# Kernel tuning notes

Measured on AMD Instinct MI355X. Metric: run time of the kernel, lower is better.

## Reference

```python
import jax, jax.numpy as jnp
import numpy as np

B, N, C, K3, KNN = 4, 4096, 128, 3, 16
SCALE = 1.0 / np.sqrt(C)  # attention uses sqrt(embed_dim)
EPS = 1e-5


def _knn_idx(x, k):
    # squared euclidean distances (monotone in cdist), topk smallest
    x2 = jnp.sum(x * x, axis=-1)                       # [B,N]
    d2 = x2[:, :, None] + x2[:, None, :] - 2.0 * jnp.einsum('bnd,bmd->bnm', x, x)
    _, idx = jax.lax.top_k(-d2, k)                     # [B,N,k]
    return idx


def _gather(x, idx):
    # knn_gather: x [B,N,D], idx [B,N,k] -> [B,N,k,D]
    return jax.vmap(lambda xb, ib: xb[ib])(x, idx)


def _attn(q_in, kv_in, Wq, Wk, Wv):
    # q_in [B,N,D], kv_in [B,N,k,D]; torch Linear: x @ W.T
    Q = q_in @ Wq.T
    Kt = kv_in @ Wk.T
    V = kv_in @ Wv.T
    scores = jnp.einsum('bnkd,bnd->bnk', Kt, Q) * SCALE
    a = jax.nn.softmax(scores, axis=-1)
    return jnp.einsum('bnk,bnkd->bnd', a, V)


def _ln(x, g, b):
    mu = jnp.mean(x, axis=-1, keepdims=True)
    var = jnp.mean((x - mu) ** 2, axis=-1, keepdims=True)
    return (x - mu) * jax.lax.rsqrt(var + EPS) * g + b


def setup_inputs() -> dict:
    key = jax.random.key(0)
    ks = jax.random.split(key, 20)
    s = 0.05
    inp = {
        'src': jax.random.normal(ks[0], (B, N, K3), dtype=jnp.float32),
        'tgt': jax.random.normal(ks[1], (B, N, C), dtype=jnp.float32),
        'Wq0': jax.random.normal(ks[2], (C, C), dtype=jnp.float32) * s,
        'Wk0': jax.random.normal(ks[3], (C, C), dtype=jnp.float32) * s,
        'Wv0': jax.random.normal(ks[4], (C, C), dtype=jnp.float32) * s,
        'Wq1': jax.random.normal(ks[5], (C, C), dtype=jnp.float32) * s,
        'Wk1': jax.random.normal(ks[6], (C, C), dtype=jnp.float32) * s,
        'Wv1': jax.random.normal(ks[7], (C, C), dtype=jnp.float32) * s,
        'Wp0': jax.random.normal(ks[8], (C, K3), dtype=jnp.float32) * s,
        'bp0': jnp.zeros((C,), dtype=jnp.float32),
        'Wp1': jax.random.normal(ks[9], (C, C), dtype=jnp.float32) * s,
        'bp1': jnp.zeros((C,), dtype=jnp.float32),
        'Wl': jax.random.normal(ks[10], (C, C), dtype=jnp.float32) * s,
        'bl': jnp.zeros((C,), dtype=jnp.float32),
        'g0': jnp.ones((C,), dtype=jnp.float32),
        'b0': jnp.zeros((C,), dtype=jnp.float32),
        'g1': jnp.ones((C,), dtype=jnp.float32),
        'b1': jnp.zeros((C,), dtype=jnp.float32),
    }
    return inp


def reference(src, tgt, Wq0, Wk0, Wv0, Wq1, Wk1, Wv1, Wp0, bp0, Wp1, bp1, Wl, bl, g0, b0, g1, b1):
    k = min(KNN, src.shape[1])
    # stage 1: knn on coordinates
    idx = _knn_idx(src, k)
    gather_src = _gather(src, idx)                         # [B,N,k,3]
    residual_src = (src[:, :, None, :] - gather_src) @ Wp0.T + bp0
    gather_tgt = _gather(tgt, idx)                         # [B,N,k,C]
    out = _attn(tgt, residual_src + gather_tgt, Wq0, Wk0, Wv0)
    # stage 2: knn in feature space
    idx2 = _knn_idx(out, k)
    gather_out = _gather(out, idx2)
    residual_out = (out[:, :, None, :] - gather_out) @ Wp1.T + bp1
    out = _attn(out, residual_out + gather_out, Wq1, Wk1, Wv1)
    out_0 = tgt + out
    out_1 = _ln(out_0, g0, b0) @ Wl.T + bl
    out_2 = _ln(tgt + out_1, g1, b1)
    return jnp.transpose(out_2, (1, 0, 2))                 # [N,B,C]
```

## Files before the change

kernel.cpp:

```cpp
#include <hip/hip_runtime.h>
#include <math.h>

#define NB 4
#define NN 4096
#define NC 128
#define NROWS (NB*NN)
#define SCALE_F 0.08838834764831845f

using bf16x8 = __attribute__((ext_vector_type(8))) short;
using f32x4  = __attribute__((ext_vector_type(4))) float;

__device__ __forceinline__ float rl_f(float x, int l) {
    return __int_as_float(__builtin_amdgcn_readlane(__float_as_int(x), l));
}
__device__ __forceinline__ ushort f2bf(float x) {
    unsigned u = __float_as_uint(x);
    return (ushort)((u + 0x7FFF + ((u >> 16) & 1)) >> 16);
}
__device__ __forceinline__ float bf2f(ushort b) { return __uint_as_float(((unsigned)b) << 16); }

__device__ __forceinline__ unsigned long long mkkey(float d2, int idx) {
    unsigned u = __float_as_uint(d2);
    u ^= ((unsigned)((int)u >> 31)) | 0x80000000u;
    return ((unsigned long long)u << 32) | (unsigned)idx;
}

#define DECL16V \
    float v0=INFINITY,v1=INFINITY,v2=INFINITY,v3=INFINITY,v4=INFINITY,v5=INFINITY,v6=INFINITY,v7=INFINITY, \
          v8=INFINITY,v9=INFINITY,v10=INFINITY,v11=INFINITY,v12=INFINITY,v13=INFINITY,v14=INFINITY,v15=INFINITY;

#define INSERT16V(dv) do { float d_=(dv); \
    bool m0=d_<v0,m1=d_<v1,m2=d_<v2,m3=d_<v3,m4=d_<v4,m5=d_<v5,m6=d_<v6,m7=d_<v7, \
         m8=d_<v8,m9=d_<v9,m10=d_<v10,m11=d_<v11,m12=d_<v12,m13=d_<v13,m14=d_<v14,m15=d_<v15; \
    v15=m14?v14:(m15?d_:v15); v14=m13?v13:(m14?d_:v14); v13=m12?v12:(m13?d_:v13); v12=m11?v11:(m12?d_:v12); \
    v11=m10?v10:(m11?d_:v11); v10=m9?v9:(m10?d_:v10); v9 =m8?v8:(m9?d_:v9);  v8 =m7?v7:(m8?d_:v8); \
    v7 =m6?v6:(m7?d_:v7);   v6 =m5?v5:(m6?d_:v6);   v5 =m4?v4:(m5?d_:v5);  v4 =m3?v3:(m4?d_:v4); \
    v3 =m2?v2:(m3?d_:v3);   v2 =m1?v1:(m2?d_:v2);   v1 =m0?v0:(m1?d_:v1);  v0 =m0?d_:v0; } while(0)

#define POP16V(p) do { bool p_=(p); \
    v0=p_?v1:v0; v1=p_?v2:v1; v2=p_?v3:v2; v3=p_?v4:v3; v4=p_?v5:v4; v5=p_?v6:v5; v6=p_?v7:v6; v7=p_?v8:v7; \
    v8=p_?v9:v8; v9=p_?v10:v9; v10=p_?v11:v10; v11=p_?v12:v11; v12=p_?v13:v12; v13=p_?v14:v13; v14=p_?v15:v14; \
    v15=p_?INFINITY:v15; } while(0)

#define KMAX16 0xFFFFFFFFFFFFFFFFull
#define DECL16K \
    unsigned long long K0=KMAX16,K1=KMAX16,K2=KMAX16,K3=KMAX16,K4=KMAX16,K5=KMAX16,K6=KMAX16,K7=KMAX16, \
                       K8=KMAX16,K9=KMAX16,K10=KMAX16,K11=KMAX16,K12=KMAX16,K13=KMAX16,K14=KMAX16,K15=KMAX16;

#define INSERT16K(kv) do { unsigned long long k_=(kv); \
    bool m0=k_<K0,m1=k_<K1,m2=k_<K2,m3=k_<K3,m4=k_<K4,m5=k_<K5,m6=k_<K6,m7=k_<K7, \
         m8=k_<K8,m9=k_<K9,m10=k_<K10,m11=k_<K11,m12=k_<K12,m13=k_<K13,m14=k_<K14,m15=k_<K15; \
    K15=m14?K14:(m15?k_:K15); K14=m13?K13:(m14?k_:K14); K13=m12?K12:(m13?k_:K13); K12=m11?K11:(m12?k_:K12); \
    K11=m10?K10:(m11?k_:K11); K10=m9?K9:(m10?k_:K10);   K9 =m8?K8:(m9?k_:K9);    K8 =m7?K7:(m8?k_:K8); \
    K7 =m6?K6:(m7?k_:K7);     K6 =m5?K5:(m6?k_:K6);     K5 =m4?K4:(m5?k_:K5);    K4 =m3?K3:(m4?k_:K4); \
    K3 =m2?K2:(m3?k_:K3);     K2 =m1?K1:(m2?k_:K2);     K1 =m0?K0:(m1?k_:K1);    K0 =m0?k_:K0; } while(0)

#define POP16K(p) do { bool p_=(p); \
    K0=p_?K1:K0; K1=p_?K2:K1; K2=p_?K3:K2; K3=p_?K4:K3; K4=p_?K5:K4; K5=p_?K6:K5; K6=p_?K7:K6; K7=p_?K8:K7; \
    K8=p_?K9:K8; K9=p_?K10:K9; K10=p_?K11:K10; K11=p_?K12:K11; K12=p_?K13:K12; K13=p_?K14:K13; K14=p_?K15:K14; \
    K15=p_?KMAX16:K15; } while(0)

__global__ void combo_small(const float* __restrict__ Wk0, const float* __restrict__ Wv0,
                            const float* __restrict__ Wp0, const float* __restrict__ bp0,
                            float* __restrict__ WKP0, float* __restrict__ BK0,
                            float* __restrict__ WVP0, float* __restrict__ BV0)
{
    int task = blockIdx.x * 512 + threadIdx.x;
    if (task >= 1024) return;
    int mat = task >> 9; int rem = task & 511;
    int c = rem >> 2, t = rem & 3;
    const float* W = mat ? Wv0 : Wk0;
    float s = 0.f;
    if (t < 3) {
        for (int d = 0; d < 128; ++d) s = fmaf(W[c*128+d], Wp0[d*3+t], s);
        (mat ? WVP0 : WKP0)[c*3+t] = s;
    } else {
        for (int d = 0; d < 128; ++d) s = fmaf(W[c*128+d], bp0[d], s);
        (mat ? BV0 : BK0)[c] = s;
    }
}

__global__ void combo_big(const float* __restrict__ Wk1, const float* __restrict__ Wv1,
                          const float* __restrict__ Wp1, const float* __restrict__ bp1,
                          float* __restrict__ WKD, float* __restrict__ MV1,
                          float* __restrict__ WVD, float* __restrict__ BV1)
{
    int task = blockIdx.x * 256 + threadIdx.x;
    if (task >= 32896) return;
    if (task < 32768) {
        int mat = task >> 14; int rem = task & 16383;
        int c = rem >> 7, tcol = rem & 127;
        const float* W = mat ? Wv1 : Wk1;
        float s = 0.f;
        for (int d = 0; d < 128; ++d) s = fmaf(W[c*128+d], Wp1[d*128+tcol], s);
        if (mat) { MV1[rem] = s; WVD[rem] = Wv1[rem] - s; }
        else     { WKD[rem] = Wk1[rem] - s; }
    } else {
        int c = task - 32768;
        float s = 0.f;
        for (int d = 0; d < 128; ++d) s = fmaf(Wv1[c*128+d], bp1[d], s);
        BV1[c] = s;
    }
}

__global__ void srcproj(const float* __restrict__ src, const float* __restrict__ WKP0,
                        const float* __restrict__ WVP0,
                        float* __restrict__ srcKp, float* __restrict__ srcVp)
{
    int gid = blockIdx.x * 256 + threadIdx.x;
    int i = gid >> 7, c = gid & 127;
    float s0 = src[i*3+0], s1 = src[i*3+1], s2 = src[i*3+2];
    srcKp[gid] = fmaf(s0, WKP0[c*3+0], fmaf(s1, WKP0[c*3+1], s2*WKP0[c*3+2]));
    srcVp[gid] = fmaf(s0, WVP0[c*3+0], fmaf(s1, WVP0[c*3+1], s2*WVP0[c*3+2]));
}

__global__ __launch_bounds__(256) void knn1_kernel(const float* __restrict__ src,
                                                   int* __restrict__ idxout)
{
    int lane = threadIdx.x & 63, wave = threadIdx.x >> 6;
    int b7 = blockIdx.x & 7, sub = blockIdx.x >> 3;
    int batch = b7 >> 1;
    int rib = (sub*2 + (b7 & 1))*4 + wave;
    int row = batch*NN + rib;
    const float* sb = src + batch*NN*3;
    float xi0 = sb[rib*3], xi1 = sb[rib*3+1], xi2 = sb[rib*3+2];

    DECL16V
    for (int it = 0; it < 64; ++it) {
        int j = it*64 + lane;
        float dx = xi0 - sb[j*3], dy = xi1 - sb[j*3+1], dz = xi2 - sb[j*3+2];
        float d2 = fmaf(dx, dx, fmaf(dy, dy, dz*dz));
        if (d2 < v15) INSERT16V(d2);
    }
    float T = INFINITY;
    for (int t = 0; t < 16; ++t) {
        float g = v0;
#pragma unroll
        for (int off = 1; off < 64; off <<= 1) g = fminf(g, __shfl_xor(g, off, 64));
        unsigned long long b = __ballot(v0 == g);
        int f = __ffsll((long long)b) - 1;
        POP16V(lane == f);
        T = g;
    }
    unsigned long long below_mask = (lane == 63) ? 0x7fffffffffffffffull : ((1ull << lane) - 1ull);
    int base = 0;
    for (int it = 0; it < 64; ++it) {
        int j = it*64 + lane;
        float dx = xi0 - sb[j*3], dy = xi1 - sb[j*3+1], dz = xi2 - sb[j*3+2];
        float d2 = fmaf(dx, dx, fmaf(dy, dy, dz*dz));
        unsigned long long blt = __ballot(d2 < T);
        if (d2 < T) idxout[row*16 + base + __popcll(blt & below_mask)] = j;
        base += __popcll(blt);
    }
    for (int it = 0; it < 64 && base < 16; ++it) {
        int j = it*64 + lane;
        float dx = xi0 - sb[j*3], dy = xi1 - sb[j*3+1], dz = xi2 - sb[j*3+2];
        float d2 = fmaf(dx, dx, fmaf(dy, dy, dz*dz));
        unsigned long long beq = __ballot(d2 == T);
        int bel = __popcll(beq & below_mask);
        if (d2 == T && base + bel < 16) idxout[row*16 + base + bel] = j;
        base += __popcll(beq);
    }
}

__device__ __forceinline__ void matmul128_body(const float* __restrict__ X,
                                               const float* __restrict__ W,
                                               const float* __restrict__ S,
                                               float* __restrict__ Y)
{
    __shared__ float WL[128*128];
    int tid = threadIdx.x;
    for (int f = tid; f < 16384; f += 256) {
        int c = f >> 7, d = f & 127;
        WL[d*128 + (c ^ (d & 14))] = W[f];
    }
    __syncthreads();
    int lane = tid & 63, wave = tid >> 6;
#pragma unroll
    for (int it = 0; it < 2; ++it) {
        int row0 = blockIdx.x*32 + it*16 + wave*4;
        float x0[4], x1[4];
#pragma unroll
        for (int r = 0; r < 4; ++r) {
            x0[r] = X[(row0+r)*128 + lane];
            x1[r] = X[(row0+r)*128 + lane + 64];
        }
        float2 acc[4];
#pragma unroll
        for (int r = 0; r < 4; ++r) { acc[r].x = 0.f; acc[r].y = 0.f; }
#pragma unroll 8
        for (int d = 0; d < 64; ++d) {
            int cidx = (2*lane) ^ (d & 14);
            float2 wa = *(const float2*)&WL[d*128 + cidx];
            float2 wb = *(const float2*)&WL[(d+64)*128 + cidx];
#pragma unroll
            for (int r = 0; r < 4; ++r) {
                float xa = rl_f(x0[r], d);
                float xb = rl_f(x1[r], d);
                acc[r].x = fmaf(xa, wa.x, acc[r].x);
                acc[r].y = fmaf(xa, wa.y, acc[r].y);
                acc[r].x = fmaf(xb, wb.x, acc[r].x);
                acc[r].y = fmaf(xb, wb.y, acc[r].y);
            }
        }
#pragma unroll
        for (int r = 0; r < 4; ++r) {
            float2 o = acc[r];
            if (S != nullptr) {
                float2 s2 = *(const float2*)&S[(row0+r)*128 + 2*lane];
                o.x -= s2.x; o.y -= s2.y;
            }
            *(float2*)&Y[(row0+r)*128 + 2*lane] = o;
        }
    }
}

__global__ __launch_bounds__(256) void matmul128x3s(
    const float* __restrict__ X,
    const float* __restrict__ W0, const float* __restrict__ W1, const float* __restrict__ W2,
    const float* __restrict__ S1, const float* __restrict__ S2,
    float* __restrict__ Y0, float* __restrict__ Y1, float* __restrict__ Y2)
{
    if (blockIdx.y == 0)      matmul128_body(X, W0, nullptr, Y0);
    else if (blockIdx.y == 1) matmul128_body(X, W1, S1, Y1);
    else                      matmul128_body(X, W2, S2, Y2);
}

__global__ __launch_bounds__(256) void matmul128x4(
    const float* __restrict__ X,
    const float* __restrict__ W0, const float* __restrict__ W1,
    const float* __restrict__ W2, const float* __restrict__ W3,
    float* __restrict__ Y0, float* __restrict__ Y1,
    float* __restrict__ Y2, float* __restrict__ Y3)
{
    const float* W; float* Y;
    switch (blockIdx.y) {
        case 0: W = W0; Y = Y0; break;
        case 1: W = W1; Y = Y1; break;
        case 2: W = W2; Y = Y2; break;
        default: W = W3; Y = Y3; break;
    }
    matmul128_body(X, W, nullptr, Y);
}

__global__ __launch_bounds__(256) void attn_kernel(
    const float* __restrict__ Q,  const float* __restrict__ GK, const float* __restrict__ GV,
    const float* __restrict__ BASE, const float* __restrict__ bv,
    const int* __restrict__ idx, float* __restrict__ outp, float* __restrict__ x2out,
    ushort* __restrict__ xh, ushort* __restrict__ xl)
{
    int lane = threadIdx.x & 63, wave = threadIdx.x >> 6;
    int b7 = blockIdx.x & 7, sub = blockIdx.x >> 3;
    int batch = b7 >> 1;
    int rib = (sub*2 + (b7 & 1))*4 + wave;
    int row = batch*NN + rib;
    const float* GKb = GK + (size_t)batch*NN*NC;
    const float* GVb = GV + (size_t)batch*NN*NC;

    float q0 = Q[row*NC + lane], q1 = Q[row*NC + lane + 64];

    int jarr[16];
#pragma unroll
    for (int k = 0; k < 16; ++k) jarr[k] = idx[row*16 + k];

    float sc[16];
#pragma unroll
    for (int k = 0; k < 16; ++k) {
        int j = jarr[k];
        float p = fmaf(q0, GKb[j*NC + lane], q1*GKb[j*NC + lane + 64]);
#pragma unroll
        for (int off = 1; off < 64; off <<= 1) p += __shfl_xor(p, off, 64);
        sc[k] = p * SCALE_F;
    }
    float m = sc[0];
#pragma unroll
    for (int k = 1; k < 16; ++k) m = fmaxf(m, sc[k]);
    float wsum = 0.f, w[16];
#pragma unroll
    for (int k = 0; k < 16; ++k) { w[k] = expf(sc[k] - m); wsum += w[k]; }
    float inv = 1.f / wsum;
    float a0 = 0.f, a1 = 0.f;
#pragma unroll
    for (int k = 0; k < 16; ++k) {
        int j = jarr[k];
        float a = w[k] * inv;
        a0 = fmaf(a, GVb[j*NC + lane],      a0);
        a1 = fmaf(a, GVb[j*NC + lane + 64], a1);
    }
    a0 += BASE[row*NC + lane]      + bv[lane];
    a1 += BASE[row*NC + lane + 64] + bv[lane + 64];
    outp[row*NC + lane]      = a0;
    outp[row*NC + lane + 64] = a1;
    if (x2out != nullptr) {
        float x2 = fmaf(a0, a0, a1*a1);
#pragma unroll
        for (int off = 1; off < 64; off <<= 1) x2 += __shfl_xor(x2, off, 64);
        if (lane == 0) x2out[row] = x2;
    }
    if (xh != nullptr) {
        ushort h0 = f2bf(a0), h1 = f2bf(a1);
        xh[row*NC + lane]      = h0;
        xh[row*NC + lane + 64] = h1;
        xl[row*NC + lane]      = f2bf(a0 - bf2f(h0));
        xl[row*NC + lane + 64] = f2bf(a1 - bf2f(h1));
    }
}

#define SCAN_STEP(CP, X2S, REFRESH) do { \
    float4 dd = *(const float4*)&DT[dtrd]; \
    float4 xx = *(const float4*)&(X2S)[slotl*4]; \
    int cb = 0; \
    { float d2 = fmaf(-2.f, dd.x, xx.x); bool p = d2 <= Trow; \
      unsigned long long bal = __ballot(p); unsigned grp = (unsigned)(bal >> grpsh) & 0xFFFFu; \
      if (p) BUF[srow][cb + __popc(grp & lowm)] = mkkey(d2, (CP) + slotl*4 + 0); \
      cb += __popc(grp); } \
    { float d2 = fmaf(-2.f, dd.y, xx.y); bool p = d2 <= Trow; \
      unsigned long long bal = __ballot(p); unsigned grp = (unsigned)(bal >> grpsh) & 0xFFFFu; \
      if (p) BUF[srow][cb + __popc(grp & lowm)] = mkkey(d2, (CP) + slotl*4 + 1); \
      cb += __popc(grp); } \
    { float d2 = fmaf(-2.f, dd.z, xx.z); bool p = d2 <= Trow; \
      unsigned long long bal = __ballot(p); unsigned grp = (unsigned)(bal >> grpsh) & 0xFFFFu; \
      if (p) BUF[srow][cb + __popc(grp & lowm)] = mkkey(d2, (CP) + slotl*4 + 2); \
      cb += __popc(grp); } \
    { float d2 = fmaf(-2.f, dd.w, xx.w); bool p = d2 <= Trow; \
      unsigned long long bal = __ballot(p); unsigned grp = (unsigned)(bal >> grpsh) & 0xFFFFu; \
      if (p) BUF[srow][cb + __popc(grp & lowm)] = mkkey(d2, (CP) + slotl*4 + 3); \
      cb += __popc(grp); } \
    _Pragma("unroll") \
    for (int r = 0; r < 4; ++r) { \
        int ii = r*16 + slotl; \
        if (ii < cb) { \
            unsigned long long k = BUF[srow][ii]; \
            if (k < K15) INSERT16K(k); \
        } \
    } \
    if (REFRESH) { \
        unsigned long long tk = K15; \
        _Pragma("unroll") \
        for (int off = 1; off < 16; off <<= 1) { \
            unsigned long long o = __shfl_xor(tk, off, 64); \
            tk = (o < tk) ? o : tk; \
        } \
        unsigned uu = (unsigned)(tk >> 32); \
        uu = (uu > 0xFF800000u) ? 0xFF800000u : uu; \
        uu = (uu & 0x80000000u) ? (uu ^ 0x80000000u) : ~uu; \
        Trow = __uint_as_float(uu); \
    } \
} while (0)

__global__ __launch_bounds__(512, 2) void knn2_kernel(const ushort* __restrict__ XHg,
                                                      const ushort* __restrict__ XLg,
                                                      const float* __restrict__ x2g,
                                                      int* __restrict__ idxout)
{
    __shared__ __align__(16) ushort XCH[64*128];
    __shared__ __align__(16) ushort XCL[64*128];
    __shared__ __align__(16) float  DT[32*64];
    __shared__ unsigned long long   BUF[32][65];
    __shared__ __align__(16) float  X2T[2][64];
    int tid = threadIdx.x;
    int lane = tid & 63, wave = tid >> 6;
    int xcd = blockIdx.x & 7, sub = blockIdx.x >> 3;
    int batch = xcd >> 1;
    int band = sub*2 + (xcd & 1);
    const ushort* XHb = XHg + (size_t)batch*NN*NC;
    const ushort* XLb = XLg + (size_t)batch*NN*NC;
    const float*  x2b = x2g + (size_t)batch*NN;
    int r0 = band*32;

    int rowblk = wave & 1, colblk = wave >> 1;
    int dbase = (lane >> 4) * 8;
    int gr = r0 + rowblk*16 + (lane & 15);
    bf16x8 AH[4], AL[4];
#pragma unroll
    for (int ks = 0; ks < 4; ++ks) {
        AH[ks] = *(const bf16x8*)&XHb[(size_t)gr*NC + ks*32 + dbase];
        AL[ks] = *(const bf16x8*)&XLb[(size_t)gr*NC + ks*32 + dbase];
    }
    int cB = colblk*16 + (lane & 15);
    int colw = colblk*16 + (lane & 15);

    int srow = tid >> 4, slotl = tid & 15;
    int grpsh = lane & 48;
    unsigned lowm = (1u << slotl) - 1u;
    int dtrd = srow*64 + ((slotl*4 + 4*srow) & 63);
    float Trow = INFINITY;
    DECL16K

    for (int t = 0; t < 64; ++t) {
        int c0 = t*64;
        __syncthreads();
#pragma unroll
        for (int i = 0; i < 2; ++i) {
            int qq = tid + 512*i;
            int c = qq >> 4, d8 = qq & 15;
            int widx = c*128 + ((d8*8) ^ ((c & 7) << 3));
            *(uint4*)&XCH[widx] = *(const uint4*)&XHb[(size_t)(c0 + c)*NC + d8*8];
            *(uint4*)&XCL[widx] = *(const uint4*)&XLb[(size_t)(c0 + c)*NC + d8*8];
        }
        if (tid < 64) X2T[t & 1][tid] = x2b[c0 + tid];
        if (t > 0) {
            const float* x2s = X2T[(t - 1) & 1];
            SCAN_STEP(c0 - 64, x2s, 1);
        }
        __syncthreads();
        f32x4 acc = {0.f, 0.f, 0.f, 0.f};
#pragma unroll
        for (int ks = 0; ks < 4; ++ks) {
            int bidx = cB*128 + ((ks*32 + dbase) ^ ((cB & 7) << 3));
            bf16x8 bh = *(const bf16x8*)&XCH[bidx];
            bf16x8 bl = *(const bf16x8*)&XCL[bidx];
            acc = __builtin_amdgcn_mfma_f32_16x16x32_bf16(AH[ks], bh, acc, 0, 0, 0);
            acc = __builtin_amdgcn_mfma_f32_16x16x32_bf16(AL[ks], bh, acc, 0, 0, 0);
            acc = __builtin_amdgcn_mfma_f32_16x16x32_bf16(AH[ks], bl, acc, 0, 0, 0);
        }
#pragma unroll
        for (int r2 = 0; r2 < 4; ++r2) {
            int rA = rowblk*16 + (lane >> 4)*4 + r2;
            DT[rA*64 + (((colw & ~3) + 4*rA) & 63) + (colw & 3)] = acc[r2];
        }
    }
    __syncthreads();
    {
        const float* x2s = X2T[1];
        SCAN_STEP(63*64, x2s, 0);
    }
    int grow = batch*NN + r0 + srow;
    for (int tt = 0; tt < 16; ++tt) {
        unsigned long long g = K0;
#pragma unroll
        for (int off = 1; off < 16; off <<= 1) {
            unsigned long long o = __shfl_xor(g, off, 64);
            g = (o < g) ? o : g;
        }
        bool win = (K0 == g);
        if (win) idxout[grow*16 + tt] = (int)(unsigned)(g & 0xFFFFFFFFull);
        POP16K(win);
    }
}

__global__ __launch_bounds__(256) void final_kernel(
    const float* __restrict__ tgt, const float* __restrict__ att,
    const float* __restrict__ Wl, const float* __restrict__ bl,
    const float* __restrict__ g0, const float* __restrict__ b0,
    const float* __restrict__ g1, const float* __restrict__ b1,
    float* __restrict__ outp)
{
    __shared__ float WL[128*128];
    int tid = threadIdx.x;
    for (int f = tid; f < 16384; f += 256) {
        int c = f >> 7, d = f & 127;
        WL[d*128 + (c ^ (d & 14))] = Wl[f];
    }
    __syncthreads();
    int lane = tid & 63, wave = tid >> 6;
    float2 gg0 = *(const float2*)&g0[2*lane];
    float2 bb0 = *(const float2*)&b0[2*lane];
    float2 gg1 = *(const float2*)&g1[2*lane];
    float2 bb1 = *(const float2*)&b1[2*lane];
    float2 bl2 = *(const float2*)&bl[2*lane];
    for (int it = 0; it < 4; ++it) {
        int row0 = blockIdx.x*64 + it*16 + wave*4;
        float2 tg[4];
        float lnx[4], lny[4];
#pragma unroll
        for (int r = 0; r < 4; ++r) {
            int row = row0 + r;
            tg[r] = *(const float2*)&tgt[row*128 + 2*lane];
            float2 at = *(const float2*)&att[row*128 + 2*lane];
            float ox = tg[r].x + at.x, oy = tg[r].y + at.y;
            float s = ox + oy;
#pragma unroll
            for (int off = 1; off < 64; off <<= 1) s += __shfl_xor(s, off, 64);
            float mu = s * (1.f/128.f);
            float dx = ox - mu, dy = oy - mu;
            float vv = fmaf(dx, dx, dy*dy);
#pragma unroll
            for (int off = 1; off < 64; off <<= 1) vv += __shfl_xor(vv, off, 64);
            float rstd = rsqrtf(vv * (1.f/128.f) + 1e-5f);
            lnx[r] = dx * rstd * gg0.x + bb0.x;
            lny[r] = dy * rstd * gg0.y + bb0.y;
        }
        float2 acc[4];
#pragma unroll
        for (int r = 0; r < 4; ++r) { acc[r].x = 0.f; acc[r].y = 0.f; }
#pragma unroll 8
        for (int dh = 0; dh < 64; ++dh) {
            int cidx = (2*lane) ^ ((2*dh) & 14);
            float2 wa = *(const float2*)&WL[(2*dh)*128 + cidx];
            float2 wb = *(const float2*)&WL[(2*dh+1)*128 + cidx];
#pragma unroll
            for (int r = 0; r < 4; ++r) {
                float xa = rl_f(lnx[r], dh);
                float xb = rl_f(lny[r], dh);
                acc[r].x = fmaf(xa, wa.x, acc[r].x);
                acc[r].y = fmaf(xa, wa.y, acc[r].y);
                acc[r].x = fmaf(xb, wb.x, acc[r].x);
                acc[r].y = fmaf(xb, wb.y, acc[r].y);
            }
        }
#pragma unroll
        for (int r = 0; r < 4; ++r) {
            int row = row0 + r;
            float zx = tg[r].x + acc[r].x + bl2.x;
            float zy = tg[r].y + acc[r].y + bl2.y;
            float s = zx + zy;
#pragma unroll
            for (int off = 1; off < 64; off <<= 1) s += __shfl_xor(s, off, 64);
            float mu = s * (1.f/128.f);
            float dx = zx - mu, dy = zy - mu;
            float vv = fmaf(dx, dx, dy*dy);
#pragma unroll
            for (int off = 1; off < 64; off <<= 1) vv += __shfl_xor(vv, off, 64);
            float rstd = rsqrtf(vv * (1.f/128.f) + 1e-5f);
            float2 res;
            res.x = dx * rstd * gg1.x + bb1.x;
            res.y = dy * rstd * gg1.y + bb1.y;
            int b = row >> 12, n = row & 4095;
            *(float2*)&outp[((size_t)n*NB + b)*128 + 2*lane] = res;
        }
    }
}

extern "C" void kernel_launch(void* const* d_in, const int* in_sizes, int n_in,
                              void* d_out, int out_size, void* d_ws, size_t ws_size,
                              hipStream_t stream)
{
    (void)in_sizes; (void)n_in; (void)out_size; (void)ws_size;
    const float* src = (const float*)d_in[0];
    const float* tgt = (const float*)d_in[1];
    const float* Wq0 = (const float*)d_in[2];
    const float* Wk0 = (const float*)d_in[3];
    const float* Wv0 = (const float*)d_in[4];
    const float* Wq1 = (const float*)d_in[5];
    const float* Wk1 = (const float*)d_in[6];
    const float* Wv1 = (const float*)d_in[7];
    const float* Wp0 = (const float*)d_in[8];
    const float* bp0 = (const float*)d_in[9];
    const float* Wp1 = (const float*)d_in[10];
    const float* bp1 = (const float*)d_in[11];
    const float* Wl  = (const float*)d_in[12];
    const float* bl  = (const float*)d_in[13];
    const float* g0  = (const float*)d_in[14];
    const float* b0  = (const float*)d_in[15];
    const float* g1  = (const float*)d_in[16];
    const float* b1  = (const float*)d_in[17];
    float* out = (float*)d_out;

    float* A0   = (float*)d_ws;
    float* A1   = A0 + 2097152;
    float* A2   = A1 + 2097152;
    float* A3   = A2 + 2097152;
    float* A4   = A3 + 2097152;
    float* OUT1 = A4 + 2097152;
    int*   IDX1 = (int*)(OUT1 + 2097152);
    int*   IDX2 = IDX1 + NROWS*16;
    float* X2G  = (float*)(IDX2 + NROWS*16);
    float* WKP0 = X2G + NROWS;
    float* BK0  = WKP0 + 384;
    float* WVP0 = BK0 + 128;
    float* BV0  = WVP0 + 384;
    float* WKD  = BV0 + 128;
    float* MV1  = WKD + 16384;
    float* WVD  = MV1 + 16384;
    float* BV1  = WVD + 16384;
    ushort* XH  = (ushort*)(BV1 + 128);
    ushort* XL  = XH + (size_t)NROWS*NC;

    combo_small<<<dim3(2), dim3(512), 0, stream>>>(Wk0, Wv0, Wp0, bp0, WKP0, BK0, WVP0, BV0);
    combo_big<<<dim3(129), dim3(256), 0, stream>>>(Wk1, Wv1, Wp1, bp1, WKD, MV1, WVD, BV1);
    srcproj<<<dim3(8192), dim3(256), 0, stream>>>(src, WKP0, WVP0, A3, A4);
    knn1_kernel<<<dim3(4096), dim3(256), 0, stream>>>(src, IDX1);
    matmul128x3s<<<dim3(512, 3), dim3(256), 0, stream>>>(tgt, Wq0, Wk0, Wv0, A3, A4, A0, A1, A2);
    attn_kernel<<<dim3(4096), dim3(256), 0, stream>>>(A0, A1, A2, A4, BV0, IDX1, OUT1, X2G, XH, XL);
    knn2_kernel<<<dim3(512), dim3(512), 0, stream>>>(XH, XL, X2G, IDX2);
    matmul128x4<<<dim3(512, 4), dim3(256), 0, stream>>>(OUT1, Wq1, WKD, WVD, MV1, A0, A1, A2, A3);
    attn_kernel<<<dim3(4096), dim3(256), 0, stream>>>(A0, A1, A2, A3, BV1, IDX2, OUT1, nullptr, nullptr, nullptr);
    final_kernel<<<dim3(256), dim3(256), 0, stream>>>(tgt, OUT1, Wl, bl, g0, b0, g1, b1, out);
}
```

Baseline: 500.5 us.

## Restructure attention to 16 lanes per row with float4 gathers; pair matmul X loads

The attention kernel now gives each row to 16 lanes, each holding 8 contiguous channels. Neighbour rows are gathered with float4 loads, the neighbour indices are broadcast by shuffle, and the dot-product reductions need only 4 shuffle steps instead of 6. The launch uses 512-thread blocks covering 32 rows each. Separately, the matmul body loads X as interleaved float2 pairs and walks the weight rows in even/odd order, halving the number of X load instructions. The aim is fewer memory transactions and fewer cross-lane reductions in this gather-bound stage, at the cost of more registers per thread and a new row-to-block mapping that must still cover every row.

After: 499.9 us. Within noise of the previous version (-0.1%).

```diff
diff --git a/kernel.cpp b/kernel.cpp
--- a/kernel.cpp
+++ b/kernel.cpp
@@ -179,24 +179,23 @@
 #pragma unroll
     for (int it = 0; it < 2; ++it) {
         int row0 = blockIdx.x*32 + it*16 + wave*4;
-        float x0[4], x1[4];
+        float2 xp[4];
 #pragma unroll
         for (int r = 0; r < 4; ++r) {
-            x0[r] = X[(row0+r)*128 + lane];
-            x1[r] = X[(row0+r)*128 + lane + 64];
+            xp[r] = *(const float2*)&X[(row0+r)*128 + 2*lane];
         }
         float2 acc[4];
 #pragma unroll
         for (int r = 0; r < 4; ++r) { acc[r].x = 0.f; acc[r].y = 0.f; }
 #pragma unroll 8
-        for (int d = 0; d < 64; ++d) {
-            int cidx = (2*lane) ^ (d & 14);
-            float2 wa = *(const float2*)&WL[d*128 + cidx];
-            float2 wb = *(const float2*)&WL[(d+64)*128 + cidx];
+        for (int dh = 0; dh < 64; ++dh) {
+            int cidx = (2*lane) ^ ((2*dh) & 14);
+            float2 wa = *(const float2*)&WL[(2*dh)*128 + cidx];
+            float2 wb = *(const float2*)&WL[(2*dh+1)*128 + cidx];
 #pragma unroll
             for (int r = 0; r < 4; ++r) {
-                float xa = rl_f(x0[r], d);
-                float xb = rl_f(x1[r], d);
+                float xa = rl_f(xp[r].x, dh);
+                float xb = rl_f(xp[r].y, dh);
                 acc[r].x = fmaf(xa, wa.x, acc[r].x);
                 acc[r].y = fmaf(xa, wa.y, acc[r].y);
                 acc[r].x = fmaf(xb, wb.x, acc[r].x);
@@ -243,33 +242,41 @@
     matmul128_body(X, W, nullptr, Y);
 }
 
-__global__ __launch_bounds__(256) void attn_kernel(
+__global__ __launch_bounds__(512) void attn_kernel(
     const float* __restrict__ Q,  const float* __restrict__ GK, const float* __restrict__ GV,
     const float* __restrict__ BASE, const float* __restrict__ bv,
     const int* __restrict__ idx, float* __restrict__ outp, float* __restrict__ x2out,
     ushort* __restrict__ xh, ushort* __restrict__ xl)
 {
-    int lane = threadIdx.x & 63, wave = threadIdx.x >> 6;
-    int b7 = blockIdx.x & 7, sub = blockIdx.x >> 3;
-    int batch = b7 >> 1;
-    int rib = (sub*2 + (b7 & 1))*4 + wave;
+    int tid = threadIdx.x;
+    int lane = tid & 63, wave = tid >> 6;
+    int xcd = blockIdx.x & 7, sub = blockIdx.x >> 3;
+    int batch = xcd >> 1;
+    int band = sub*2 + (xcd & 1);
+    int rgrp = lane >> 4;
+    int dimg = lane & 15;
+    int rib = band*32 + wave*4 + rgrp;
     int row = batch*NN + rib;
+    int d0 = dimg*8;
+    int gbase = lane & 48;
     const float* GKb = GK + (size_t)batch*NN*NC;
     const float* GVb = GV + (size_t)batch*NN*NC;
 
-    float q0 = Q[row*NC + lane], q1 = Q[row*NC + lane + 64];
-
-    int jarr[16];
-#pragma unroll
-    for (int k = 0; k < 16; ++k) jarr[k] = idx[row*16 + k];
+    float4 q0 = *(const float4*)&Q[(size_t)row*NC + d0];
+    float4 q1 = *(const float4*)&Q[(size_t)row*NC + d0 + 4];
+    int jv = idx[row*16 + dimg];
 
     float sc[16];
 #pragma unroll
     for (int k = 0; k < 16; ++k) {
-        int j = jarr[k];
-        float p = fmaf(q0, GKb[j*NC + lane], q1*GKb[j*NC + lane + 64]);
-#pragma unroll
-        for (int off = 1; off < 64; off <<= 1) p += __shfl_xor(p, off, 64);
+        int j = __shfl(jv, gbase + k, 64);
+        const float* gk = &GKb[(size_t)j*NC + d0];
+        float4 g0 = *(const float4*)gk;
+        float4 g1 = *(const float4*)(gk + 4);
+        float p = fmaf(q0.x, g0.x, fmaf(q0.y, g0.y, fmaf(q0.z, g0.z, fmaf(q0.w, g0.w,
+                  fmaf(q1.x, g1.x, fmaf(q1.y, g1.y, fmaf(q1.z, g1.z, q1.w*g1.w)))))));
+#pragma unroll
+        for (int off = 1; off < 16; off <<= 1) p += __shfl_xor(p, off, 64);
         sc[k] = p * SCALE_F;
     }
     float m = sc[0];
@@ -279,30 +286,55 @@
 #pragma unroll
     for (int k = 0; k < 16; ++k) { w[k] = expf(sc[k] - m); wsum += w[k]; }
     float inv = 1.f / wsum;
-    float a0 = 0.f, a1 = 0.f;
+
+    float4 a0 = {0.f,0.f,0.f,0.f}, a1 = {0.f,0.f,0.f,0.f};
 #pragma unroll
     for (int k = 0; k < 16; ++k) {
-        int j = jarr[k];
+        int j = __shfl(jv, gbase + k, 64);
+        const float* gv = &GVb[(size_t)j*NC + d0];
+        float4 v0 = *(const float4*)gv;
+        float4 v1 = *(const float4*)(gv + 4);
         float a = w[k] * inv;
-        a0 = fmaf(a, GVb[j*NC + lane],      a0);
-        a1 = fmaf(a, GVb[j*NC + lane + 64], a1);
-    }
-    a0 += BASE[row*NC + lane]      + bv[lane];
-    a1 += BASE[row*NC + lane + 64] + bv[lane + 64];
-    outp[row*NC + lane]      = a0;
-    outp[row*NC + lane + 64] = a1;
+        a0.x = fmaf(a, v0.x, a0.x); a0.y = fmaf(a, v0.y, a0.y);
+        a0.z = fmaf(a, v0.z, a0.z); a0.w = fmaf(a, v0.w, a0.w);
+        a1.x = fmaf(a, v1.x, a1.x); a1.y = fmaf(a, v1.y, a1.y);
+        a1.z = fmaf(a, v1.z, a1.z); a1.w = fmaf(a, v1.w, a1.w);
+    }
+    float4 b0 = *(const float4*)&BASE[(size_t)row*NC + d0];
+    float4 b1 = *(const float4*)&BASE[(size_t)row*NC + d0 + 4];
+    float4 c0 = *(const float4*)&bv[d0];
+    float4 c1 = *(const float4*)&bv[d0 + 4];
+    a0.x += b0.x + c0.x; a0.y += b0.y + c0.y; a0.z += b0.z + c0.z; a0.w += b0.w + c0.w;
+    a1.x += b1.x + c1.x; a1.y += b1.y + c1.y; a1.z += b1.z + c1.z; a1.w += b1.w + c1.w;
+    *(float4*)&outp[(size_t)row*NC + d0]     = a0;
+    *(float4*)&outp[(size_t)row*NC + d0 + 4] = a1;
+
     if (x2out != nullptr) {
-        float x2 = fmaf(a0, a0, a1*a1);
-#pragma unroll
-        for (int off = 1; off < 64; off <<= 1) x2 += __shfl_xor(x2, off, 64);
-        if (lane == 0) x2out[row] = x2;
+        float x2 = fmaf(a0.x, a0.x, fmaf(a0.y, a0.y, fmaf(a0.z, a0.z, fmaf(a0.w, a0.w,
+                   fmaf(a1.x, a1.x, fmaf(a1.y, a1.y, fmaf(a1.z, a1.z, a1.w*a1.w)))))));
+#pragma unroll
+        for (int off = 1; off < 16; off <<= 1) x2 += __shfl_xor(x2, off, 64);
+        if (dimg == 0) x2out[row] = x2;
     }
     if (xh != nullptr) {
-        ushort h0 = f2bf(a0), h1 = f2bf(a1);
-        xh[row*NC + lane]      = h0;
-        xh[row*NC + lane + 64] = h1;
-        xl[row*NC + lane]      = f2bf(a0 - bf2f(h0));
-        xl[row*NC + lane + 64] = f2bf(a1 - bf2f(h1));
+        ushort h0 = f2bf(a0.x), h1 = f2bf(a0.y), h2 = f2bf(a0.z), h3 = f2bf(a0.w);
+        ushort h4 = f2bf(a1.x), h5 = f2bf(a1.y), h6 = f2bf(a1.z), h7 = f2bf(a1.w);
+        uint4 ph;
+        ph.x = (unsigned)h0 | ((unsigned)h1 << 16);
+        ph.y = (unsigned)h2 | ((unsigned)h3 << 16);
+        ph.z = (unsigned)h4 | ((unsigned)h5 << 16);
+        ph.w = (unsigned)h6 | ((unsigned)h7 << 16);
+        *(uint4*)&xh[(size_t)row*NC + d0] = ph;
+        ushort l0 = f2bf(a0.x - bf2f(h0)), l1 = f2bf(a0.y - bf2f(h1));
+        ushort l2 = f2bf(a0.z - bf2f(h2)), l3 = f2bf(a0.w - bf2f(h3));
+        ushort l4 = f2bf(a1.x - bf2f(h4)), l5 = f2bf(a1.y - bf2f(h5));
+        ushort l6 = f2bf(a1.z - bf2f(h6)), l7 = f2bf(a1.w - bf2f(h7));
+        uint4 pl;
+        pl.x = (unsigned)l0 | ((unsigned)l1 << 16);
+        pl.y = (unsigned)l2 | ((unsigned)l3 << 16);
+        pl.z = (unsigned)l4 | ((unsigned)l5 << 16);
+        pl.w = (unsigned)l6 | ((unsigned)l7 << 16);
+        *(uint4*)&xl[(size_t)row*NC + d0] = pl;
     }
 }
 
@@ -572,9 +604,9 @@
     srcproj<<<dim3(8192), dim3(256), 0, stream>>>(src, WKP0, WVP0, A3, A4);
     knn1_kernel<<<dim3(4096), dim3(256), 0, stream>>>(src, IDX1);
     matmul128x3s<<<dim3(512, 3), dim3(256), 0, stream>>>(tgt, Wq0, Wk0, Wv0, A3, A4, A0, A1, A2);
-    attn_kernel<<<dim3(4096), dim3(256), 0, stream>>>(A0, A1, A2, A4, BV0, IDX1, OUT1, X2G, XH, XL);
+    attn_kernel<<<dim3(512), dim3(512), 0, stream>>>(A0, A1, A2, A4, BV0, IDX1, OUT1, X2G, XH, XL);
     knn2_kernel<<<dim3(512), dim3(512), 0, stream>>>(XH, XL, X2G, IDX2);
     matmul128x4<<<dim3(512, 4), dim3(256), 0, stream>>>(OUT1, Wq1, WKD, WVD, MV1, A0, A1, A2, A3);
-    attn_kernel<<<dim3(4096), dim3(256), 0, stream>>>(A0, A1, A2, A3, BV1, IDX2, OUT1, nullptr, nullptr, nullptr);
+    attn_kernel<<<dim3(512), dim3(512), 0, stream>>>(A0, A1, A2, A3, BV1, IDX2, OUT1, nullptr, nullptr, nullptr);
     final_kernel<<<dim3(256), dim3(256), 0, stream>>>(tgt, OUT1, Wl, bl, g0, b0, g1, b1, out);
 }
```
